# Optimization experiments

Hardware: AMD Instinct MI355X
Metric: run time of the kernel (lower is better)

## Reference

```python
import jax, jax.numpy as jnp
import numpy as np

B, T, D, H = 4, 1024, 1024, 16
HD = D // H  # 64
EPS = 1e-5


def _layernorm(x, g, b):
    mu = jnp.mean(x, axis=-1, keepdims=True)
    var = jnp.mean(jnp.square(x - mu), axis=-1, keepdims=True)
    return (x - mu) * jax.lax.rsqrt(var + EPS) * g + b


def _apply_rope(x, cos, sin):
    # x: (B, H, T, HD); cos/sin: (T, HD//2)
    d = x.shape[-1] // 2
    x1, x2 = x[..., :d], x[..., d:]
    cos = cos[None, None]
    sin = sin[None, None]
    return jnp.concatenate([x1 * cos - x2 * sin, x1 * sin + x2 * cos], axis=-1)


def setup_inputs() -> dict:
    key = jax.random.key(0)
    ks = jax.random.split(key, 8)
    s = 0.02
    x = jax.random.normal(ks[0], (B, T, D), jnp.float32)
    # RoPE tables
    pos = jnp.arange(T, dtype=jnp.float32)
    inv_freq = 1.0 / (10000.0 ** (jnp.arange(HD // 2, dtype=jnp.float32) / (HD // 2)))
    ang = pos[:, None] * inv_freq[None, :]  # (T, HD//2)
    rope_cos, rope_sin = jnp.cos(ang), jnp.sin(ang)
    # causal mask: True = masked out (module does ~attn_mask before SDPA)
    attn_mask = jnp.triu(jnp.ones((T, T), dtype=bool), k=1)
    params = dict(
        ln1_g=jnp.ones((D,), jnp.float32), ln1_b=jnp.zeros((D,), jnp.float32),
        w_qkv=jax.random.normal(ks[1], (D, 3 * D), jnp.float32) * s,
        b_qkv=jnp.zeros((3 * D,), jnp.float32),
        w_out=jax.random.normal(ks[2], (D, D), jnp.float32) * s,
        b_out=jnp.zeros((D,), jnp.float32),
        ln2_g=jnp.ones((D,), jnp.float32), ln2_b=jnp.zeros((D,), jnp.float32),
        w1=jax.random.normal(ks[3], (D, 4 * D), jnp.float32) * s,
        b1=jnp.zeros((4 * D,), jnp.float32),
        w2=jax.random.normal(ks[4], (4 * D, D), jnp.float32) * s,
        b2=jnp.zeros((D,), jnp.float32),
    )
    return dict(x=x, attn_mask=attn_mask, rope_cos=rope_cos, rope_sin=rope_sin, **params)


def reference(x, attn_mask, rope_cos, rope_sin, ln1_g, ln1_b, w_qkv, b_qkv,
              w_out, b_out, ln2_g, ln2_b, w1, b1, w2, b2):
    b, t, d = x.shape
    h = _layernorm(x, ln1_g, ln1_b)
    qkv = (h @ w_qkv + b_qkv).reshape(b, t, 3, H, HD)
    q, k, v = jnp.transpose(qkv, (2, 0, 3, 1, 4))  # each (B, H, T, HD)
    q = _apply_rope(q, rope_cos, rope_sin)
    k = _apply_rope(k, rope_cos, rope_sin)
    scale = 1.0 / jnp.sqrt(jnp.asarray(HD, x.dtype))
    scores = jnp.einsum('bhqd,bhkd->bhqk', q, k) * scale
    allowed = ~attn_mask  # True = attend
    neg = jnp.finfo(scores.dtype).min
    scores = jnp.where(allowed[None, None], scores, neg)
    probs = jax.nn.softmax(scores, axis=-1)
    attn = jnp.einsum('bhqk,bhkd->bhqd', probs, v)
    attn = jnp.transpose(attn, (0, 2, 1, 3)).reshape(b, t, d)
    x = x + (attn @ w_out + b_out)
    h2 = _layernorm(x, ln2_g, ln2_b)
    mlp = jax.nn.gelu(h2 @ w1 + b1, approximate=False) @ w2 + b2
    return x + mlp
```

## Files before the change

kernel.cpp:

```cpp
#include <hip/hip_runtime.h>
#include <hip/hip_bf16.h>
#include <cstdint>


typedef __bf16 bf16x8_t __attribute__((ext_vector_type(8)));
typedef float  f32x4_t  __attribute__((ext_vector_type(4)));

#define MFMA16(a, b, c) __builtin_amdgcn_mfma_f32_16x16x32_bf16((a), (b), (c), 0, 0, 0)

static constexpr int Bb = 4, T = 1024, D = 1024, NH = 16, HD = 64;
static constexpr int ROWS = Bb * T;
static constexpr int QKVN = 3 * D;

__device__ __forceinline__ float bf2f(__hip_bfloat16 v) { return __bfloat162float(v); }
__device__ __forceinline__ ushort f2bfbits(float v) {
    __hip_bfloat16 h = __float2bfloat16(v);
    return *reinterpret_cast<ushort*>(&h);
}
__device__ __forceinline__ float loadf(const void* p, size_t i, int isb16) {
    return isb16 ? bf2f(((const __hip_bfloat16*)p)[i]) : ((const float*)p)[i];
}
__device__ __forceinline__ int dtype16(const void* gref) {
    return (((const unsigned*)gref)[0] & 0xFFFFu) != 0u;
}
__device__ __forceinline__ void gld_lds16(const __hip_bfloat16* g, __hip_bfloat16* l) {
    __builtin_amdgcn_global_load_lds(
        (const __attribute__((address_space(1))) void*)g,
        (__attribute__((address_space(3))) void*)l, 16, 0, 0);
}

__device__ __forceinline__ void trans_tile(const void* B, __hip_bfloat16* BT,
                                           int K, int N, int k0, int n0, int isb16) {
    __shared__ ushort t[64][65];
#pragma unroll
    for (int it = 0; it < 16; ++it) {
        int idx = threadIdx.x + it * 256;
        int r = idx >> 6, c = idx & 63;
        t[c][r] = f2bfbits(loadf(B, (size_t)(k0 + r) * N + n0 + c, isb16));
    }
    __syncthreads();
#pragma unroll
    for (int it = 0; it < 16; ++it) {
        int idx = threadIdx.x + it * 256;
        int r = idx >> 6, c = idx & 63;
        reinterpret_cast<ushort*>(BT)[(size_t)(n0 + r) * K + k0 + c] = t[r][c];
    }
}

__global__ __launch_bounds__(256) void transpose_k(const void* __restrict__ B,
                                                   __hip_bfloat16* __restrict__ BT,
                                                   const void* __restrict__ gref,
                                                   int K, int N) {
    trans_tile(B, BT, K, N, blockIdx.y * 64, blockIdx.x * 64, dtype16(gref));
}

__global__ __launch_bounds__(256) void megatrans_k(const void* w_qkv, const void* w_out,
                                                   const void* w1, const void* w2,
                                                   __hip_bfloat16* wqkvT, __hip_bfloat16* woutT,
                                                   __hip_bfloat16* w1T, __hip_bfloat16* w2T,
                                                   const void* __restrict__ gref) {
    const int isb16 = dtype16(gref);
    int bid = blockIdx.x;
    const void* src; __hip_bfloat16* dst; int K, N, l;
    if (bid < 768)       { src = w_qkv; dst = wqkvT; K = 1024; N = 3072; l = bid; }
    else if (bid < 1024) { src = w_out; dst = woutT; K = 1024; N = 1024; l = bid - 768; }
    else if (bid < 2048) { src = w1;    dst = w1T;   K = 1024; N = 4096; l = bid - 1024; }
    else                 { src = w2;    dst = w2T;   K = 4096; N = 1024; l = bid - 2048; }
    const int nb = N / 64;
    trans_tile(src, dst, K, N, (l / nb) * 64, (l % nb) * 64, isb16);
}

__global__ __launch_bounds__(256) void ln_k(const void* __restrict__ x,
                                            const void* __restrict__ g,
                                            const void* __restrict__ bt,
                                            __hip_bfloat16* __restrict__ out,
                                            const void* __restrict__ gref) {
    const int isb16 = dtype16(gref);
    const int row = blockIdx.x, tid = threadIdx.x;
    const int lane = tid & 63, w = tid >> 6;

    float v[4];
    if (isb16) {
        ushort4 raw = reinterpret_cast<const ushort4*>((const __hip_bfloat16*)x + (size_t)row * D)[tid];
        v[0] = __uint_as_float(((unsigned)raw.x) << 16);
        v[1] = __uint_as_float(((unsigned)raw.y) << 16);
        v[2] = __uint_as_float(((unsigned)raw.z) << 16);
        v[3] = __uint_as_float(((unsigned)raw.w) << 16);
    } else {
        float4 f = reinterpret_cast<const float4*>((const float*)x + (size_t)row * D)[tid];
        v[0] = f.x; v[1] = f.y; v[2] = f.z; v[3] = f.w;
    }

    float s1 = v[0] + v[1] + v[2] + v[3];
    float s2 = v[0] * v[0] + v[1] * v[1] + v[2] * v[2] + v[3] * v[3];
#pragma unroll
    for (int off = 32; off >= 1; off >>= 1) {
        s1 += __shfl_xor(s1, off, 64);
        s2 += __shfl_xor(s2, off, 64);
    }
    __shared__ float r1[4], r2[4];
    if (lane == 0) { r1[w] = s1; r2[w] = s2; }
    __syncthreads();
    float t1 = r1[0] + r1[1] + r1[2] + r1[3];
    float t2 = r2[0] + r2[1] + r2[2] + r2[3];
    float mu  = t1 * (1.0f / D);
    float var = t2 * (1.0f / D) - mu * mu;
    float rstd = rsqrtf(var + 1e-5f);

    const int c = tid * 4;
#pragma unroll
    for (int j = 0; j < 4; j++) {
        float gv = loadf(g, c + j, isb16), bv = loadf(bt, c + j, isb16);
        out[(size_t)row * D + c + j] = __float2bfloat16((v[j] - mu) * rstd * gv + bv);
    }
}

template <int MODE, bool SPLIT>
__global__ __launch_bounds__(256) void gemm_k(const __hip_bfloat16* __restrict__ A,
                                              const __hip_bfloat16* __restrict__ BT,
                                              const void* __restrict__ bias,
                                              void* __restrict__ C,
                                              const void* __restrict__ gref,
                                              int M, int N, int Kstride, int klen) {
    __shared__ __hip_bfloat16 As[2][2][128 * 32];
    __shared__ __hip_bfloat16 Bs[2][2][128 * 32];

    const int tid  = threadIdx.x;
    const int lane = tid & 63, w = tid >> 6;
    const int quad = lane >> 4, l15 = lane & 15;
    const int n0 = blockIdx.x * 128, m0 = blockIdx.y * 128;
    const int wm = (w >> 1) * 64, wn = (w & 1) * 64;
    const int kbase = SPLIT ? blockIdx.z * klen : 0;

    const int srow = lane >> 2, skk = (lane & 3) * 8;
    const __hip_bfloat16* Ag = A  + (size_t)(m0 + w * 32 + srow) * Kstride + kbase + skk;
    const __hip_bfloat16* Bg = BT + (size_t)(n0 + w * 32 + srow) * Kstride + kbase + skk;
    const int lb0 = (w * 32) * 32, lb1 = (w * 32 + 16) * 32;

    f32x4_t acc[4][4] = {};

#pragma unroll
    for (int kk = 0; kk < 2; kk++) {
        gld_lds16(Ag + kk * 32,                &As[0][kk][lb0]);
        gld_lds16(Ag + kk * 32 + 16 * Kstride, &As[0][kk][lb1]);
        gld_lds16(Bg + kk * 32,                &Bs[0][kk][lb0]);
        gld_lds16(Bg + kk * 32 + 16 * Kstride, &Bs[0][kk][lb1]);
    }
    __syncthreads();

    int p = 0;
    for (int k0 = 0; k0 < klen; k0 += 64) {
        if (k0 + 64 < klen) {
#pragma unroll
            for (int kk = 0; kk < 2; kk++) {
                gld_lds16(Ag + k0 + 64 + kk * 32,                &As[p ^ 1][kk][lb0]);
                gld_lds16(Ag + k0 + 64 + kk * 32 + 16 * Kstride, &As[p ^ 1][kk][lb1]);
                gld_lds16(Bg + k0 + 64 + kk * 32,                &Bs[p ^ 1][kk][lb0]);
                gld_lds16(Bg + k0 + 64 + kk * 32 + 16 * Kstride, &Bs[p ^ 1][kk][lb1]);
            }
        }

#pragma unroll
        for (int kk = 0; kk < 2; kk++) {
            bf16x8_t af[4], bfr[4];
#pragma unroll
            for (int t = 0; t < 4; t++) {
                af[t]  = *reinterpret_cast<const bf16x8_t*>(&As[p][kk][(wm + t * 16 + l15) * 32 + quad * 8]);
                bfr[t] = *reinterpret_cast<const bf16x8_t*>(&Bs[p][kk][(wn + t * 16 + l15) * 32 + quad * 8]);
            }
#pragma unroll
            for (int i = 0; i < 4; i++)
#pragma unroll
                for (int j = 0; j < 4; j++)
                    acc[i][j] = MFMA16(af[i], bfr[j], acc[i][j]);
        }

        __syncthreads();
        p ^= 1;
    }

    __hip_bfloat16* Cb = (__hip_bfloat16*)C;
    if constexpr (SPLIT) Cb += (size_t)blockIdx.z * M * N;
    const int isb16 = (MODE == 3) ? 0 : dtype16(gref);
    __hip_bfloat16* E = &As[0][0][0];
#pragma unroll
    for (int j = 0; j < 4; j++) {
        const int cc = wn + j * 16 + l15;
        const float bsv = (MODE == 3) ? 0.0f : loadf(bias, n0 + cc, isb16);
#pragma unroll
        for (int i = 0; i < 4; i++) {
            const int rbase = wm + i * 16 + quad * 4;
#pragma unroll
            for (int r = 0; r < 4; r++) {
                const int rr = rbase + r;
                float v = acc[i][j][r] + bsv;
                if constexpr (MODE == 2)
                    v = 0.5f * v * (1.0f + erff(v * 0.70710678118654752f));
                E[rr * 128 + ((cc + (((rr >> 2) & 7) << 4)) & 127)] = __float2bfloat16(v);
            }
        }
    }
    __syncthreads();
#pragma unroll
    for (int it = 0; it < 8; it++) {
        const int r = it * 16 + (tid >> 4), c = (tid & 15) * 8;
        const int cs = (c + (((r >> 2) & 7) << 4)) & 127;
        uint4 d = *reinterpret_cast<const uint4*>(&E[r * 128 + cs]);
        *reinterpret_cast<uint4*>(&Cb[(size_t)(m0 + r) * N + n0 + c]) = d;
    }
}

__global__ __launch_bounds__(256) void reduce_k(const __hip_bfloat16* __restrict__ p0,
                                                const __hip_bfloat16* __restrict__ p1,
                                                const void* __restrict__ bias,
                                                const void* __restrict__ res,
                                                void* __restrict__ out,
                                                const void* __restrict__ gref) {
    const int isb16 = dtype16(gref);
    const size_t i = ((size_t)blockIdx.x * 256 + threadIdx.x) * 4;
    ushort4 a = *reinterpret_cast<const ushort4*>(p0 + i);
    ushort4 b = *reinterpret_cast<const ushort4*>(p1 + i);
    const int col = (int)(i & (D - 1));
    float v[4];
    v[0] = __uint_as_float((unsigned)a.x << 16) + __uint_as_float((unsigned)b.x << 16);
    v[1] = __uint_as_float((unsigned)a.y << 16) + __uint_as_float((unsigned)b.y << 16);
    v[2] = __uint_as_float((unsigned)a.z << 16) + __uint_as_float((unsigned)b.z << 16);
    v[3] = __uint_as_float((unsigned)a.w << 16) + __uint_as_float((unsigned)b.w << 16);
#pragma unroll
    for (int j = 0; j < 4; j++)
        v[j] += loadf(bias, col + j, isb16) + loadf(res, i + j, isb16);
    if (isb16) {
        ushort4 o;
        o.x = f2bfbits(v[0]); o.y = f2bfbits(v[1]); o.z = f2bfbits(v[2]); o.w = f2bfbits(v[3]);
        *reinterpret_cast<ushort4*>((__hip_bfloat16*)out + i) = o;
    } else {
        float4 o = {v[0], v[1], v[2], v[3]};
        *reinterpret_cast<float4*>((float*)out + i) = o;
    }
}

__global__ __launch_bounds__(256) void gemm64_k(const __hip_bfloat16* __restrict__ A,
                                                const __hip_bfloat16* __restrict__ BT,
                                                const void* __restrict__ bias,
                                                const void* __restrict__ res,
                                                void* __restrict__ C,
                                                const void* __restrict__ gref,
                                                int M, int N, int K, int crow0) {
    __shared__ __hip_bfloat16 As[2][2][128 * 32];
    __shared__ __hip_bfloat16 Bs[2][2][64 * 32];

    const int tid  = threadIdx.x;
    const int lane = tid & 63, w = tid >> 6;
    const int quad = lane >> 4, l15 = lane & 15;
    const int n0 = blockIdx.x * 64, m0 = blockIdx.y * 128;
    const int wm = (w >> 1) * 64, wn = (w & 1) * 32;

    const int srow = lane >> 2, skk = (lane & 3) * 8;
    const __hip_bfloat16* Ag = A  + (size_t)(m0 + w * 32 + srow) * K + skk;
    const __hip_bfloat16* Bg = BT + (size_t)(n0 + w * 16 + srow) * K + skk;
    const int alb0 = (w * 32) * 32, alb1 = (w * 32 + 16) * 32;
    const int blb  = (w * 16) * 32;

    f32x4_t acc[4][2] = {};

#pragma unroll
    for (int kk = 0; kk < 2; kk++) {
        gld_lds16(Ag + kk * 32,          &As[0][kk][alb0]);
        gld_lds16(Ag + kk * 32 + 16 * K, &As[0][kk][alb1]);
        gld_lds16(Bg + kk * 32,          &Bs[0][kk][blb]);
    }
    __syncthreads();

    int p = 0;
    for (int k0 = 0; k0 < K; k0 += 64) {
        if (k0 + 64 < K) {
#pragma unroll
            for (int kk = 0; kk < 2; kk++) {
                gld_lds16(Ag + k0 + 64 + kk * 32,          &As[p ^ 1][kk][alb0]);
                gld_lds16(Ag + k0 + 64 + kk * 32 + 16 * K, &As[p ^ 1][kk][alb1]);
                gld_lds16(Bg + k0 + 64 + kk * 32,          &Bs[p ^ 1][kk][blb]);
            }
        }

#pragma unroll
        for (int kk = 0; kk < 2; kk++) {
            bf16x8_t af[4], bfr[2];
#pragma unroll
            for (int t = 0; t < 4; t++)
                af[t]  = *reinterpret_cast<const bf16x8_t*>(&As[p][kk][(wm + t * 16 + l15) * 32 + quad * 8]);
#pragma unroll
            for (int t = 0; t < 2; t++)
                bfr[t] = *reinterpret_cast<const bf16x8_t*>(&Bs[p][kk][(wn + t * 16 + l15) * 32 + quad * 8]);
#pragma unroll
            for (int i = 0; i < 4; i++)
#pragma unroll
                for (int j = 0; j < 2; j++)
                    acc[i][j] = MFMA16(af[i], bfr[j], acc[i][j]);
        }

        __syncthreads();
        p ^= 1;
    }

    const int isb16 = dtype16(gref);
#pragma unroll
    for (int j = 0; j < 2; j++) {
        const int col = n0 + wn + j * 16 + l15;
        const float bsv = loadf(bias, col, isb16);
#pragma unroll
        for (int i = 0; i < 4; i++) {
            const int rbase = m0 + wm + i * 16 + quad * 4;
#pragma unroll
            for (int r = 0; r < 4; r++) {
                const size_t gr = (size_t)(crow0 + rbase + r);
                float v = acc[i][j][r] + bsv + loadf(res, gr * N + col, isb16);
                if (isb16) ((__hip_bfloat16*)C)[gr * N + col] = __float2bfloat16(v);
                else       ((float*)C)[gr * N + col] = v;
            }
        }
    }
}

__global__ __launch_bounds__(256) void ropevt_k(__hip_bfloat16* __restrict__ qkv,
                                                const void* __restrict__ rc,
                                                const void* __restrict__ rs,
                                                __hip_bfloat16* __restrict__ vT,
                                                const void* __restrict__ gref) {
    const int bid = blockIdx.x;
    if (bid < 8192) {
        const int isb16 = dtype16(gref);
        const int id = bid * 256 + threadIdx.x;
        const int d  = id & 31;
        const int h  = (id >> 5) & 15;
        const int t  = (id >> 9) & 1023;
        const int b  = id >> 19;
        const float c = loadf(rc, t * 32 + d, isb16);
        const float s = loadf(rs, t * 32 + d, isb16);
        __hip_bfloat16* base = qkv + ((size_t)(b * T + t)) * QKVN + h * HD + d;
        float x1 = bf2f(base[0]), x2 = bf2f(base[32]);
        base[0]  = __float2bfloat16((x1 * c - x2 * s) * 0.125f);
        base[32] = __float2bfloat16((x1 * s + x2 * c) * 0.125f);
        float y1 = bf2f(base[D]), y2 = bf2f(base[D + 32]);
        base[D]      = __float2bfloat16(y1 * c - y2 * s);
        base[D + 32] = __float2bfloat16(y1 * s + y2 * c);
    } else {
        __shared__ ushort t[64][65];
        const int l = bid - 8192;
        const int t0 = (l & 15) * 64, bh = l >> 4;
        const int b = bh >> 4, h = bh & 15;
        const __hip_bfloat16* src = qkv + ((size_t)b * T) * QKVN + 2 * D + h * HD;
#pragma unroll
        for (int it = 0; it < 16; ++it) {
            int idx = threadIdx.x + it * 256;
            int r = idx >> 6, d = idx & 63;
            t[d][r] = *reinterpret_cast<const ushort*>(src + (size_t)(t0 + r) * QKVN + d);
        }
        __syncthreads();
#pragma unroll
        for (int it = 0; it < 16; ++it) {
            int idx = threadIdx.x + it * 256;
            int r = idx >> 6, c = idx & 63;
            reinterpret_cast<ushort*>(vT)[((size_t)bh * 64 + r) * T + t0 + c] = t[r][c];
        }
    }
}

__global__ __launch_bounds__(256) void flash_k(const __hip_bfloat16* __restrict__ qkv,
                                               const __hip_bfloat16* __restrict__ vT,
                                               __hip_bfloat16* __restrict__ out) {
    __shared__ __hip_bfloat16 Qs[2][64 * 32];
    __shared__ __hip_bfloat16 Ks[2][2][64 * 32];
    __shared__ __hip_bfloat16 Vs[2][2][64 * 32];
    __shared__ __hip_bfloat16 Ps[4][2][16 * 32];

    const int tid = threadIdx.x;
    const int bid = blockIdx.x;
    const int qt = 15 - (bid >> 6);
    const int bh = bid & 63;
    const int b = bh >> 4, h = bh & 15;
    const int q0 = qt * 64;
    const int lane = tid & 63, w = tid >> 6, quad = lane >> 4, l15 = lane & 15;
    const int srow = lane >> 2, skk = (lane & 3) * 8;

    const __hip_bfloat16* qg = qkv + ((size_t)(b * T) + q0 + w * 16 + srow) * QKVN + h * HD + skk;
    const __hip_bfloat16* kg = qkv + ((size_t)(b * T) + w * 16 + srow) * QKVN + D + h * HD + skk;
    const __hip_bfloat16* vg = vT + ((size_t)bh * 64 + w * 16 + srow) * T + skk;

    gld_lds16(qg,      &Qs[0][(w * 16) * 32]);
    gld_lds16(qg + 32, &Qs[1][(w * 16) * 32]);
    gld_lds16(kg,      &Ks[0][0][(w * 16) * 32]);
    gld_lds16(kg + 32, &Ks[0][1][(w * 16) * 32]);
    gld_lds16(vg,      &Vs[0][0][(w * 16) * 32]);
    gld_lds16(vg + 32, &Vs[0][1][(w * 16) * 32]);
    __syncthreads();

    const bf16x8_t aq0 = *reinterpret_cast<const bf16x8_t*>(&Qs[0][(w * 16 + l15) * 32 + quad * 8]);
    const bf16x8_t aq1 = *reinterpret_cast<const bf16x8_t*>(&Qs[1][(w * 16 + l15) * 32 + quad * 8]);

    float m_run[4], l_run[4];
    f32x4_t o[4] = {};
#pragma unroll
    for (int i = 0; i < 4; i++) { m_run[i] = -1e30f; l_run[i] = 0.0f; }

    int p = 0;
    for (int kt = 0; kt <= qt; kt++) {
        if (kt < qt) {
            const size_t ko = (size_t)(kt + 1) * 64;
            gld_lds16(kg + ko * QKVN,      &Ks[p ^ 1][0][(w * 16) * 32]);
            gld_lds16(kg + ko * QKVN + 32, &Ks[p ^ 1][1][(w * 16) * 32]);
            gld_lds16(vg + ko,             &Vs[p ^ 1][0][(w * 16) * 32]);
            gld_lds16(vg + ko + 32,        &Vs[p ^ 1][1][(w * 16) * 32]);
        }

        f32x4_t s[4];
#pragma unroll
        for (int c = 0; c < 4; c++) {
            f32x4_t z = {};
            bf16x8_t k0f = *reinterpret_cast<const bf16x8_t*>(&Ks[p][0][(c * 16 + l15) * 32 + quad * 8]);
            bf16x8_t k1f = *reinterpret_cast<const bf16x8_t*>(&Ks[p][1][(c * 16 + l15) * 32 + quad * 8]);
            z = MFMA16(aq0, k0f, z);
            z = MFMA16(aq1, k1f, z);
            s[c] = z;
        }

        if (kt == qt) {
#pragma unroll
            for (int c = 0; c < 4; c++)
#pragma unroll
                for (int i = 0; i < 4; i++) {
                    int rr = w * 16 + quad * 4 + i;
                    int cc = c * 16 + l15;
                    if (cc > rr) s[c][i] = -1e30f;
                }
        }

        float mnew[4], alpha[4];
#pragma unroll
        for (int i = 0; i < 4; i++) {
            float mx = fmaxf(fmaxf(s[0][i], s[1][i]), fmaxf(s[2][i], s[3][i]));
#pragma unroll
            for (int off = 1; off < 16; off <<= 1) mx = fmaxf(mx, __shfl_xor(mx, off, 64));
            mnew[i] = fmaxf(m_run[i], mx);
            alpha[i] = __expf(m_run[i] - mnew[i]);
            m_run[i] = mnew[i];
        }
#pragma unroll
        for (int c = 0; c < 4; c++)
#pragma unroll
            for (int i = 0; i < 4; i++) s[c][i] = __expf(s[c][i] - mnew[i]);
#pragma unroll
        for (int i = 0; i < 4; i++) {
            float sm = s[0][i] + s[1][i] + s[2][i] + s[3][i];
#pragma unroll
            for (int off = 1; off < 16; off <<= 1) sm += __shfl_xor(sm, off, 64);
            l_run[i] = l_run[i] * alpha[i] + sm;
#pragma unroll
            for (int od = 0; od < 4; od++) o[od][i] *= alpha[i];
        }

#pragma unroll
        for (int c = 0; c < 4; c++)
#pragma unroll
            for (int i = 0; i < 4; i++)
                Ps[w][c >> 1][(quad * 4 + i) * 32 + (c & 1) * 16 + l15] =
                    __float2bfloat16(s[c][i]);

        bf16x8_t ap0 = *reinterpret_cast<const bf16x8_t*>(&Ps[w][0][l15 * 32 + quad * 8]);
        bf16x8_t ap1 = *reinterpret_cast<const bf16x8_t*>(&Ps[w][1][l15 * 32 + quad * 8]);
#pragma unroll
        for (int od = 0; od < 4; od++) {
            bf16x8_t v0f = *reinterpret_cast<const bf16x8_t*>(&Vs[p][0][(od * 16 + l15) * 32 + quad * 8]);
            bf16x8_t v1f = *reinterpret_cast<const bf16x8_t*>(&Vs[p][1][(od * 16 + l15) * 32 + quad * 8]);
            o[od] = MFMA16(ap0, v0f, o[od]);
            o[od] = MFMA16(ap1, v1f, o[od]);
        }

        __syncthreads();
        p ^= 1;
    }

#pragma unroll
    for (int od = 0; od < 4; od++)
#pragma unroll
        for (int i = 0; i < 4; i++) {
            int row = q0 + w * 16 + quad * 4 + i;
            int col = h * HD + od * 16 + l15;
            float v = o[od][i] / l_run[i];
            out[((size_t)b * T + row) * D + col] = __float2bfloat16(v);
        }
}

extern "C" void kernel_launch(void* const* d_in, const int* in_sizes, int n_in,
                              void* d_out, int out_size, void* d_ws, size_t ws_size,
                              hipStream_t stream) {
    const int o = (in_sizes[1] == T * (HD / 2)) ? 1 : 2;
    const void* x     = d_in[0];
    const void* rc    = d_in[o + 0];
    const void* rs    = d_in[o + 1];
    const void* ln1g  = d_in[o + 2];
    const void* ln1b  = d_in[o + 3];
    const void* w_qkv = d_in[o + 4];
    const void* b_qkv = d_in[o + 5];
    const void* w_out = d_in[o + 6];
    const void* b_out = d_in[o + 7];
    const void* ln2g  = d_in[o + 8];
    const void* ln2b  = d_in[o + 9];
    const void* w1    = d_in[o + 10];
    const void* b1    = d_in[o + 11];
    const void* w2    = d_in[o + 12];
    const void* b2    = d_in[o + 13];

    char* ws = (char*)d_ws;
    const size_t MB = 1024 * 1024;

    if (ws_size >= 72 * MB + 256) {
        __hip_bfloat16* bufA  = (__hip_bfloat16*)(ws + 256);
        __hip_bfloat16* qkvb  = (__hip_bfloat16*)(ws + 8 * MB + 256);
        __hip_bfloat16* vTb   = (__hip_bfloat16*)(ws + 32 * MB + 256);
        __hip_bfloat16* mid   = qkvb;
        __hip_bfloat16* wqkvT = (__hip_bfloat16*)(ws + 40 * MB + 256);
        __hip_bfloat16* woutT = (__hip_bfloat16*)(ws + 46 * MB + 256);
        __hip_bfloat16* w1T   = (__hip_bfloat16*)(ws + 48 * MB + 256);
        __hip_bfloat16* w2T   = (__hip_bfloat16*)(ws + 56 * MB + 256);
        __hip_bfloat16* part0 = (__hip_bfloat16*)(ws + 40 * MB + 256);
        __hip_bfloat16* part1 = (__hip_bfloat16*)(ws + 48 * MB + 256);

        megatrans_k<<<3072, 256, 0, stream>>>(w_qkv, w_out, w1, w2,
                                              wqkvT, woutT, w1T, w2T, ln1g);
        ln_k<<<ROWS, 256, 0, stream>>>(x, ln1g, ln1b, bufA, ln1g);
        gemm_k<0, false><<<dim3(QKVN / 128, ROWS / 128), 256, 0, stream>>>(
            bufA, wqkvT, b_qkv, qkvb, ln1g, ROWS, QKVN, D, D);
        ropevt_k<<<8192 + 1024, 256, 0, stream>>>(qkvb, rc, rs, vTb, ln1g);
        flash_k<<<16 * Bb * NH, 256, 0, stream>>>(qkvb, vTb, bufA);
        gemm64_k<<<dim3(D / 64, ROWS / 128), 256, 0, stream>>>(bufA, woutT, b_out, x,
                                                               d_out, ln1g, ROWS, D, D, 0);
        ln_k<<<ROWS, 256, 0, stream>>>(d_out, ln2g, ln2b, bufA, ln1g);
        gemm_k<2, false><<<dim3(4 * D / 128, ROWS / 128), 256, 0, stream>>>(
            bufA, w1T, b1, mid, ln1g, ROWS, 4 * D, D, D);
        gemm_k<3, true><<<dim3(D / 128, ROWS / 128, 2), 256, 0, stream>>>(
            mid, w2T, nullptr, part0, ln1g, ROWS, D, 4 * D, 2 * D);
        reduce_k<<<(ROWS * D) / (256 * 4), 256, 0, stream>>>(part0, part1, b2,
                                                             d_out, d_out, ln1g);
    } else {
        __hip_bfloat16* bufA  = (__hip_bfloat16*)(ws + 256);
        __hip_bfloat16* qkvb  = (__hip_bfloat16*)(ws + 8 * MB + 256);
        __hip_bfloat16* wqkvT = (__hip_bfloat16*)(ws + 32 * MB + 256);
        __hip_bfloat16* vTb   = (__hip_bfloat16*)(ws + 32 * MB + 256);
        __hip_bfloat16* woutT = (__hip_bfloat16*)(ws + 8 * MB + 256);
        __hip_bfloat16* w1T   = (__hip_bfloat16*)(ws + 8 * MB + 256);
        __hip_bfloat16* w2T   = (__hip_bfloat16*)(ws + 16 * MB + 256);
        __hip_bfloat16* mid   = (__hip_bfloat16*)(ws + 24 * MB + 256);

        transpose_k<<<dim3(QKVN / 64, D / 64), 256, 0, stream>>>(w_qkv, wqkvT, ln1g, D, QKVN);
        ln_k<<<ROWS, 256, 0, stream>>>(x, ln1g, ln1b, bufA, ln1g);
        gemm_k<0, false><<<dim3(QKVN / 128, ROWS / 128), 256, 0, stream>>>(
            bufA, wqkvT, b_qkv, qkvb, ln1g, ROWS, QKVN, D, D);
        ropevt_k<<<8192 + 1024, 256, 0, stream>>>(qkvb, rc, rs, vTb, ln1g);
        flash_k<<<16 * Bb * NH, 256, 0, stream>>>(qkvb, vTb, bufA);
        transpose_k<<<dim3(D / 64, D / 64), 256, 0, stream>>>(w_out, woutT, ln1g, D, D);
        gemm64_k<<<dim3(D / 64, ROWS / 128), 256, 0, stream>>>(bufA, woutT, b_out, x,
                                                               d_out, ln1g, ROWS, D, D, 0);
        ln_k<<<ROWS, 256, 0, stream>>>(d_out, ln2g, ln2b, bufA, ln1g);
        transpose_k<<<dim3(4 * D / 64, D / 64), 256, 0, stream>>>(w1, w1T, ln1g, D, 4 * D);
        transpose_k<<<dim3(D / 64, 4 * D / 64), 256, 0, stream>>>(w2, w2T, ln1g, 4 * D, D);
        for (int c = 0; c < 2; c++) {
            const int ro = c * 2048;
            gemm_k<2, false><<<dim3(4 * D / 128, 2048 / 128), 256, 0, stream>>>(
                bufA + (size_t)ro * D, w1T, b1, mid, ln1g, 2048, 4 * D, D, D);
            gemm64_k<<<dim3(D / 64, 2048 / 128), 256, 0, stream>>>(mid, w2T, b2, d_out,
                                                                   d_out, ln1g, 2048, D, 4 * D, ro);
        }
    }
}
```

Before: 392.0 us.

## Halve GEMM K-tile to shrink LDS and raise MLP down-proj split-K to four

Both GEMM kernels now stage 32-wide K slices instead of 64 in one flat shared buffer. This halves LDS per block so more blocks can be resident on each CU, at the cost of twice as many barriers per K. The second MLP GEMM's split-K factor goes from 2 to 4 so more blocks run in parallel. The extra partials are written into spare workspace and the freed bufA, passed in through the unused bias and gref pointers, and a four-way reduce kernel sums them. That adds extra partial-sum memory traffic.

```diff
diff --git a/kernel.cpp b/kernel.cpp
--- a/kernel.cpp
+++ b/kernel.cpp
@@ -122,8 +122,7 @@
                                               void* __restrict__ C,
                                               const void* __restrict__ gref,
                                               int M, int N, int Kstride, int klen) {
-    __shared__ __hip_bfloat16 As[2][2][128 * 32];
-    __shared__ __hip_bfloat16 Bs[2][2][128 * 32];
+    __shared__ __hip_bfloat16 LB[16384];
 
     const int tid  = threadIdx.x;
     const int lane = tid & 63, w = tid >> 6;
@@ -133,56 +132,59 @@
     const int kbase = SPLIT ? blockIdx.z * klen : 0;
 
     const int srow = lane >> 2, skk = (lane & 3) * 8;
-    const __hip_bfloat16* Ag = A  + (size_t)(m0 + w * 32 + srow) * Kstride + kbase + skk;
-    const __hip_bfloat16* Bg = BT + (size_t)(n0 + w * 32 + srow) * Kstride + kbase + skk;
-    const int lb0 = (w * 32) * 32, lb1 = (w * 32 + 16) * 32;
+    const __hip_bfloat16* Ag = A  + (size_t)(m0 + w * 16 + srow) * Kstride + kbase + skk;
+    const __hip_bfloat16* Bg = BT + (size_t)(n0 + w * 16 + srow) * Kstride + kbase + skk;
+    const int lwb = (w * 16) * 32;
 
     f32x4_t acc[4][4] = {};
 
-#pragma unroll
-    for (int kk = 0; kk < 2; kk++) {
-        gld_lds16(Ag + kk * 32,                &As[0][kk][lb0]);
-        gld_lds16(Ag + kk * 32 + 16 * Kstride, &As[0][kk][lb1]);
-        gld_lds16(Bg + kk * 32,                &Bs[0][kk][lb0]);
-        gld_lds16(Bg + kk * 32 + 16 * Kstride, &Bs[0][kk][lb1]);
-    }
+    gld_lds16(Ag,                LB + lwb);
+    gld_lds16(Ag + 64 * Kstride, LB + lwb + 64 * 32);
+    gld_lds16(Bg,                LB + 8192 + lwb);
+    gld_lds16(Bg + 64 * Kstride, LB + 8192 + lwb + 64 * 32);
     __syncthreads();
 
     int p = 0;
-    for (int k0 = 0; k0 < klen; k0 += 64) {
-        if (k0 + 64 < klen) {
-#pragma unroll
-            for (int kk = 0; kk < 2; kk++) {
-                gld_lds16(Ag + k0 + 64 + kk * 32,                &As[p ^ 1][kk][lb0]);
-                gld_lds16(Ag + k0 + 64 + kk * 32 + 16 * Kstride, &As[p ^ 1][kk][lb1]);
-                gld_lds16(Bg + k0 + 64 + kk * 32,                &Bs[p ^ 1][kk][lb0]);
-                gld_lds16(Bg + k0 + 64 + kk * 32 + 16 * Kstride, &Bs[p ^ 1][kk][lb1]);
-            }
-        }
-
-#pragma unroll
-        for (int kk = 0; kk < 2; kk++) {
-            bf16x8_t af[4], bfr[4];
-#pragma unroll
-            for (int t = 0; t < 4; t++) {
-                af[t]  = *reinterpret_cast<const bf16x8_t*>(&As[p][kk][(wm + t * 16 + l15) * 32 + quad * 8]);
-                bfr[t] = *reinterpret_cast<const bf16x8_t*>(&Bs[p][kk][(wn + t * 16 + l15) * 32 + quad * 8]);
-            }
-#pragma unroll
-            for (int i = 0; i < 4; i++)
-#pragma unroll
-                for (int j = 0; j < 4; j++)
-                    acc[i][j] = MFMA16(af[i], bfr[j], acc[i][j]);
-        }
+    for (int k0 = 0; k0 < klen; k0 += 32) {
+        if (k0 + 32 < klen) {
+            __hip_bfloat16* An = LB + (p ^ 1) * 4096;
+            __hip_bfloat16* Bn = LB + 8192 + (p ^ 1) * 4096;
+            gld_lds16(Ag + k0 + 32,                An + lwb);
+            gld_lds16(Ag + k0 + 32 + 64 * Kstride, An + lwb + 64 * 32);
+            gld_lds16(Bg + k0 + 32,                Bn + lwb);
+            gld_lds16(Bg + k0 + 32 + 64 * Kstride, Bn + lwb + 64 * 32);
+        }
+
+        const __hip_bfloat16* Ac = LB + p * 4096;
+        const __hip_bfloat16* Bc = LB + 8192 + p * 4096;
+        bf16x8_t af[4], bfr[4];
+#pragma unroll
+        for (int t = 0; t < 4; t++) {
+            af[t]  = *reinterpret_cast<const bf16x8_t*>(&Ac[(wm + t * 16 + l15) * 32 + quad * 8]);
+            bfr[t] = *reinterpret_cast<const bf16x8_t*>(&Bc[(wn + t * 16 + l15) * 32 + quad * 8]);
+        }
+#pragma unroll
+        for (int i = 0; i < 4; i++)
+#pragma unroll
+            for (int j = 0; j < 4; j++)
+                acc[i][j] = MFMA16(af[i], bfr[j], acc[i][j]);
 
         __syncthreads();
         p ^= 1;
     }
 
-    __hip_bfloat16* Cb = (__hip_bfloat16*)C;
-    if constexpr (SPLIT) Cb += (size_t)blockIdx.z * M * N;
+    __hip_bfloat16* Cb;
+    if constexpr (SPLIT) {
+        const int z = blockIdx.z;
+        if (z == 0)      Cb = (__hip_bfloat16*)C;
+        else if (z == 1) Cb = (__hip_bfloat16*)C + (size_t)M * N;
+        else if (z == 2) Cb = (__hip_bfloat16*)const_cast<void*>(bias);
+        else             Cb = (__hip_bfloat16*)const_cast<void*>(gref);
+    } else {
+        Cb = (__hip_bfloat16*)C;
+    }
     const int isb16 = (MODE == 3) ? 0 : dtype16(gref);
-    __hip_bfloat16* E = &As[0][0][0];
+    __hip_bfloat16* E = LB;
 #pragma unroll
     for (int j = 0; j < 4; j++) {
         const int cc = wn + j * 16 + l15;
@@ -210,22 +212,30 @@
     }
 }
 
-__global__ __launch_bounds__(256) void reduce_k(const __hip_bfloat16* __restrict__ p0,
-                                                const __hip_bfloat16* __restrict__ p1,
-                                                const void* __restrict__ bias,
-                                                const void* __restrict__ res,
-                                                void* __restrict__ out,
-                                                const void* __restrict__ gref) {
+__global__ __launch_bounds__(256) void reduce4_k(const __hip_bfloat16* __restrict__ p0,
+                                                 const __hip_bfloat16* __restrict__ p1,
+                                                 const __hip_bfloat16* __restrict__ p2,
+                                                 const __hip_bfloat16* __restrict__ p3,
+                                                 const void* __restrict__ bias,
+                                                 const void* __restrict__ res,
+                                                 void* __restrict__ out,
+                                                 const void* __restrict__ gref) {
     const int isb16 = dtype16(gref);
     const size_t i = ((size_t)blockIdx.x * 256 + threadIdx.x) * 4;
     ushort4 a = *reinterpret_cast<const ushort4*>(p0 + i);
     ushort4 b = *reinterpret_cast<const ushort4*>(p1 + i);
+    ushort4 c = *reinterpret_cast<const ushort4*>(p2 + i);
+    ushort4 d = *reinterpret_cast<const ushort4*>(p3 + i);
     const int col = (int)(i & (D - 1));
     float v[4];
-    v[0] = __uint_as_float((unsigned)a.x << 16) + __uint_as_float((unsigned)b.x << 16);
-    v[1] = __uint_as_float((unsigned)a.y << 16) + __uint_as_float((unsigned)b.y << 16);
-    v[2] = __uint_as_float((unsigned)a.z << 16) + __uint_as_float((unsigned)b.z << 16);
-    v[3] = __uint_as_float((unsigned)a.w << 16) + __uint_as_float((unsigned)b.w << 16);
+    v[0] = __uint_as_float((unsigned)a.x << 16) + __uint_as_float((unsigned)b.x << 16)
+         + __uint_as_float((unsigned)c.x << 16) + __uint_as_float((unsigned)d.x << 16);
+    v[1] = __uint_as_float((unsigned)a.y << 16) + __uint_as_float((unsigned)b.y << 16)
+         + __uint_as_float((unsigned)c.y << 16) + __uint_as_float((unsigned)d.y << 16);
+    v[2] = __uint_as_float((unsigned)a.z << 16) + __uint_as_float((unsigned)b.z << 16)
+         + __uint_as_float((unsigned)c.z << 16) + __uint_as_float((unsigned)d.z << 16);
+    v[3] = __uint_as_float((unsigned)a.w << 16) + __uint_as_float((unsigned)b.w << 16)
+         + __uint_as_float((unsigned)c.w << 16) + __uint_as_float((unsigned)d.w << 16);
 #pragma unroll
     for (int j = 0; j < 4; j++)
         v[j] += loadf(bias, col + j, isb16) + loadf(res, i + j, isb16);
@@ -246,8 +256,7 @@
                                                 void* __restrict__ C,
                                                 const void* __restrict__ gref,
                                                 int M, int N, int K, int crow0) {
-    __shared__ __hip_bfloat16 As[2][2][128 * 32];
-    __shared__ __hip_bfloat16 Bs[2][2][64 * 32];
+    __shared__ __hip_bfloat16 LB64[12288];
 
     const int tid  = threadIdx.x;
     const int lane = tid & 63, w = tid >> 6;
@@ -256,47 +265,41 @@
     const int wm = (w >> 1) * 64, wn = (w & 1) * 32;
 
     const int srow = lane >> 2, skk = (lane & 3) * 8;
-    const __hip_bfloat16* Ag = A  + (size_t)(m0 + w * 32 + srow) * K + skk;
+    const __hip_bfloat16* Ag = A  + (size_t)(m0 + w * 16 + srow) * K + skk;
     const __hip_bfloat16* Bg = BT + (size_t)(n0 + w * 16 + srow) * K + skk;
-    const int alb0 = (w * 32) * 32, alb1 = (w * 32 + 16) * 32;
-    const int blb  = (w * 16) * 32;
+    const int lwb = (w * 16) * 32;
 
     f32x4_t acc[4][2] = {};
 
-#pragma unroll
-    for (int kk = 0; kk < 2; kk++) {
-        gld_lds16(Ag + kk * 32,          &As[0][kk][alb0]);
-        gld_lds16(Ag + kk * 32 + 16 * K, &As[0][kk][alb1]);
-        gld_lds16(Bg + kk * 32,          &Bs[0][kk][blb]);
-    }
+    gld_lds16(Ag,          LB64 + lwb);
+    gld_lds16(Ag + 64 * K, LB64 + lwb + 64 * 32);
+    gld_lds16(Bg,          LB64 + 8192 + lwb);
     __syncthreads();
 
     int p = 0;
-    for (int k0 = 0; k0 < K; k0 += 64) {
-        if (k0 + 64 < K) {
-#pragma unroll
-            for (int kk = 0; kk < 2; kk++) {
-                gld_lds16(Ag + k0 + 64 + kk * 32,          &As[p ^ 1][kk][alb0]);
-                gld_lds16(Ag + k0 + 64 + kk * 32 + 16 * K, &As[p ^ 1][kk][alb1]);
-                gld_lds16(Bg + k0 + 64 + kk * 32,          &Bs[p ^ 1][kk][blb]);
-            }
-        }
-
-#pragma unroll
-        for (int kk = 0; kk < 2; kk++) {
-            bf16x8_t af[4], bfr[2];
-#pragma unroll
-            for (int t = 0; t < 4; t++)
-                af[t]  = *reinterpret_cast<const bf16x8_t*>(&As[p][kk][(wm + t * 16 + l15) * 32 + quad * 8]);
-#pragma unroll
-            for (int t = 0; t < 2; t++)
-                bfr[t] = *reinterpret_cast<const bf16x8_t*>(&Bs[p][kk][(wn + t * 16 + l15) * 32 + quad * 8]);
-#pragma unroll
-            for (int i = 0; i < 4; i++)
-#pragma unroll
-                for (int j = 0; j < 2; j++)
-                    acc[i][j] = MFMA16(af[i], bfr[j], acc[i][j]);
-        }
+    for (int k0 = 0; k0 < K; k0 += 32) {
+        if (k0 + 32 < K) {
+            __hip_bfloat16* An = LB64 + (p ^ 1) * 4096;
+            __hip_bfloat16* Bn = LB64 + 8192 + (p ^ 1) * 2048;
+            gld_lds16(Ag + k0 + 32,          An + lwb);
+            gld_lds16(Ag + k0 + 32 + 64 * K, An + lwb + 64 * 32);
+            gld_lds16(Bg + k0 + 32,          Bn + lwb);
+        }
+
+        const __hip_bfloat16* Ac = LB64 + p * 4096;
+        const __hip_bfloat16* Bc = LB64 + 8192 + p * 2048;
+        bf16x8_t af[4], bfr[2];
+#pragma unroll
+        for (int t = 0; t < 4; t++)
+            af[t]  = *reinterpret_cast<const bf16x8_t*>(&Ac[(wm + t * 16 + l15) * 32 + quad * 8]);
+#pragma unroll
+        for (int t = 0; t < 2; t++)
+            bfr[t] = *reinterpret_cast<const bf16x8_t*>(&Bc[(wn + t * 16 + l15) * 32 + quad * 8]);
+#pragma unroll
+        for (int i = 0; i < 4; i++)
+#pragma unroll
+            for (int j = 0; j < 2; j++)
+                acc[i][j] = MFMA16(af[i], bfr[j], acc[i][j]);
 
         __syncthreads();
         p ^= 1;
@@ -523,7 +526,9 @@
         __hip_bfloat16* w1T   = (__hip_bfloat16*)(ws + 48 * MB + 256);
         __hip_bfloat16* w2T   = (__hip_bfloat16*)(ws + 56 * MB + 256);
         __hip_bfloat16* part0 = (__hip_bfloat16*)(ws + 40 * MB + 256);
+        __hip_bfloat16* part2 = (__hip_bfloat16*)(ws + 64 * MB + 256);
         __hip_bfloat16* part1 = (__hip_bfloat16*)(ws + 48 * MB + 256);
+        __hip_bfloat16* part3 = bufA;
 
         megatrans_k<<<3072, 256, 0, stream>>>(w_qkv, w_out, w1, w2,
                                               wqkvT, woutT, w1T, w2T, ln1g);
@@ -537,10 +542,10 @@
         ln_k<<<ROWS, 256, 0, stream>>>(d_out, ln2g, ln2b, bufA, ln1g);
         gemm_k<2, false><<<dim3(4 * D / 128, ROWS / 128), 256, 0, stream>>>(
             bufA, w1T, b1, mid, ln1g, ROWS, 4 * D, D, D);
-        gemm_k<3, true><<<dim3(D / 128, ROWS / 128, 2), 256, 0, stream>>>(
-            mid, w2T, nullptr, part0, ln1g, ROWS, D, 4 * D, 2 * D);
-        reduce_k<<<(ROWS * D) / (256 * 4), 256, 0, stream>>>(part0, part1, b2,
-                                                             d_out, d_out, ln1g);
+        gemm_k<3, true><<<dim3(D / 128, ROWS / 128, 4), 256, 0, stream>>>(
+            mid, w2T, part2, part0, part3, ROWS, D, 4 * D, D);
+        reduce4_k<<<(ROWS * D) / (256 * 4), 256, 0, stream>>>(part0, part1, part2, part3,
+                                                              b2, d_out, d_out, ln1g);
     } else {
         __hip_bfloat16* bufA  = (__hip_bfloat16*)(ws + 256);
         __hip_bfloat16* qkvb  = (__hip_bfloat16*)(ws + 8 * MB + 256);
```

Result: no change. 399.8 us (+2.0%).
